# Optimization experiments

Hardware: AMD Instinct MI355X
Metric: run time of the kernel (lower is better)

## Reference

```python
import jax, jax.numpy as jnp
import numpy as np

EPS = 1e-6
H = 16  # heads

def rmsnorm(x, w):
    return x * jax.lax.rsqrt(jnp.mean(x * x, axis=-1, keepdims=True) + EPS) * w

def l2norm(x):
    return x * jax.lax.rsqrt(jnp.sum(x * x, axis=-1, keepdims=True) + EPS)

def setup_inputs() -> dict:
    key = jax.random.key(0)
    ks = jax.random.split(key, 12)
    B, S, D, F = 2, 2048, 1024, 4096
    std = 0.02
    inp = {
        'hidden_states': jax.random.normal(ks[0], (B, S, D), jnp.float32),
        'Wq': jax.random.normal(ks[1], (D, D), jnp.float32) * std,
        'Wk': jax.random.normal(ks[2], (D, D), jnp.float32) * std,
        'Wv': jax.random.normal(ks[3], (D, D), jnp.float32) * std,
        'Wb': jax.random.normal(ks[4], (D, H), jnp.float32) * std,
        'Wo': jax.random.normal(ks[5], (D, D), jnp.float32) * std,
        'ln1': jnp.ones((D,), jnp.float32),
        'ln2': jnp.ones((D,), jnp.float32),
        'Wg': jax.random.normal(ks[6], (D, F), jnp.float32) * std,
        'Wu': jax.random.normal(ks[7], (D, F), jnp.float32) * std,
        'Wd': jax.random.normal(ks[8], (F, D), jnp.float32) * std,
    }
    return inp

def delta_rule(q, k, v, beta):
    # q,k: [B,S,H,dk] (l2-normalized), v: [B,S,H,dv], beta: [B,S,H]
    B, S, Hh, dk = q.shape
    dv = v.shape[-1]
    # time-major for scan: [S,B,H,...]
    qt = jnp.moveaxis(q, 1, 0)
    kt = jnp.moveaxis(k, 1, 0)
    vt = jnp.moveaxis(v, 1, 0)
    bt = jnp.moveaxis(beta, 1, 0)

    def step(Sm, inp):
        qi, ki, vi, bi = inp  # [B,H,dk],[B,H,dk],[B,H,dv],[B,H]
        Sk = jnp.einsum('bhkv,bhk->bhv', Sm, ki)          # S^T k
        upd = ki[..., :, None] * (vi - Sk)[..., None, :]  # outer(k, v - S^T k)
        Sm = Sm + bi[..., None, None] * upd
        oi = jnp.einsum('bhkv,bhk->bhv', Sm, qi)
        return Sm, oi

    S0 = jnp.zeros((B, Hh, dk, dv), q.dtype)
    _, out = jax.lax.scan(step, S0, (qt, kt, vt, bt))
    return jnp.moveaxis(out, 0, 1)  # [B,S,H,dv]

def reference(hidden_states, Wq, Wk, Wv, Wb, Wo, ln1, ln2, Wg, Wu, Wd):
    B, S, D = hidden_states.shape
    dk = D // H
    # --- delta-rule attention sub-block ---
    x = rmsnorm(hidden_states, ln1)
    q = l2norm(jax.nn.silu(x @ Wq).reshape(B, S, H, dk))
    k = l2norm(jax.nn.silu(x @ Wk).reshape(B, S, H, dk))
    v = jax.nn.silu(x @ Wv).reshape(B, S, H, dk)
    beta = jax.nn.sigmoid(x @ Wb)  # [B,S,H]
    o = delta_rule(q, k, v, beta).reshape(B, S, D)
    h = hidden_states + o @ Wo
    # --- SwiGLU MLP sub-block ---
    y = rmsnorm(h, ln2)
    h = h + (jax.nn.silu(y @ Wg) * (y @ Wu)) @ Wd
    return h
```

## Files before the change

### kernel.cpp

```cpp
#include <hip/hip_runtime.h>
#include <hip/hip_bf16.h>
#include <stdint.h>

#define BB 2
#define SS 2048
#define DD 1024
#define FF 4096
#define HH 16
#define ROWS (BB*SS)
#define NC 32
#define NQKV 3200

typedef float f32x4 __attribute__((ext_vector_type(4)));
typedef __bf16 bf16x8 __attribute__((ext_vector_type(8)));

typedef __attribute__((address_space(1))) const void* gas1p;
typedef __attribute__((address_space(3))) void* las3p;

__device__ __forceinline__ void gload16(const void* g, void* l) {
    __builtin_amdgcn_global_load_lds((gas1p)g, (las3p)l, 16, 0, 0);
}

__device__ __forceinline__ unsigned short f2bf(float f) {
    unsigned int u = __builtin_bit_cast(unsigned int, f);
    u += 0x7fffu + ((u >> 16) & 1u);
    return (unsigned short)(u >> 16);
}
__device__ __forceinline__ float bf2f(unsigned short s) {
    unsigned int u = ((unsigned int)s) << 16;
    return __builtin_bit_cast(float, u);
}
__device__ __forceinline__ float sigmoidf_(float x) { return 1.f / (1.f + __expf(-x)); }
__device__ __forceinline__ float siluf_(float x)    { return x / (1.f + __expf(-x)); }

__device__ __forceinline__ int swz(int b) { return b ^ (((b >> 7) & 7) << 4); }

__device__ __forceinline__ void tp_body(const float* __restrict__ W,
                                        unsigned short* __restrict__ Wt,
                                        int K, int N, int bx, int by, int tid) {
    __shared__ float tile[32][33];
    int tx = tid & 31, ty = tid >> 5;
    int n0 = bx * 32, k0 = by * 32;
#pragma unroll
    for (int i = 0; i < 4; ++i)
        tile[ty + 8 * i][tx] = W[(size_t)(k0 + ty + 8 * i) * N + n0 + tx];
    __syncthreads();
#pragma unroll
    for (int i = 0; i < 4; ++i)
        Wt[(size_t)(n0 + ty + 8 * i) * K + k0 + tx] = f2bf(tile[tx][ty + 8 * i]);
}

__global__ __launch_bounds__(256) void transpose_cvt(const float* __restrict__ W,
                                                     unsigned short* __restrict__ Wt,
                                                     int K, int N) {
    tp_body(W, Wt, K, N, blockIdx.x, blockIdx.y, threadIdx.x);
}

__global__ __launch_bounds__(256) void transpose_cvt4(const float* W0, const float* W1,
                                                      const float* W2, const float* W3,
                                                      unsigned short* T0, unsigned short* T1,
                                                      unsigned short* T2, unsigned short* T3) {
    const float* W = (blockIdx.z == 0) ? W0 : (blockIdx.z == 1) ? W1 : (blockIdx.z == 2) ? W2 : W3;
    unsigned short* T = (blockIdx.z == 0) ? T0 : (blockIdx.z == 1) ? T1 : (blockIdx.z == 2) ? T2 : T3;
    tp_body(W, T, DD, DD, blockIdx.x, blockIdx.y, threadIdx.x);
}

__global__ __launch_bounds__(256) void transpose_cvt_gu(const float* W0, const float* W1,
                                                        unsigned short* Wt) {
    const float* W = (blockIdx.z == 0) ? W0 : W1;
    int isU = blockIdx.z;
    __shared__ float tile[32][33];
    int tid = threadIdx.x;
    int tx = tid & 31, ty = tid >> 5;
    int n0 = blockIdx.x * 32, k0 = blockIdx.y * 32;
#pragma unroll
    for (int i = 0; i < 4; ++i)
        tile[ty + 8 * i][tx] = W[(size_t)(k0 + ty + 8 * i) * FF + n0 + tx];
    __syncthreads();
#pragma unroll
    for (int i = 0; i < 4; ++i) {
        int j = n0 + ty + 8 * i;
        int rint = ((j >> 4) << 5) + (j & 15) + (isU << 4);
        Wt[(size_t)rint * DD + k0 + tx] = f2bf(tile[tx][ty + 8 * i]);
    }
}

__global__ __launch_bounds__(256) void wbt_kernel(const float* __restrict__ Wb,
                                                  unsigned short* __restrict__ WbT) {
    int idx = blockIdx.x * 256 + threadIdx.x;
    int d = idx >> 4, h = idx & 15;
    WbT[h * DD + d] = f2bf(Wb[idx]);
}

__global__ __launch_bounds__(256) void rmsnorm_bf16_kernel(const float* __restrict__ src,
                                                           const float* __restrict__ w,
                                                           unsigned short* __restrict__ dst) {
    int row = blockIdx.x;
    int tid = threadIdx.x;
    float4 x = ((const float4*)(src + (size_t)row * DD))[tid];
    float ss = x.x * x.x + x.y * x.y + x.z * x.z + x.w * x.w;
#pragma unroll
    for (int m = 1; m < 64; m <<= 1) ss += __shfl_xor(ss, m, 64);
    __shared__ float ws4[4];
    if ((tid & 63) == 0) ws4[tid >> 6] = ss;
    __syncthreads();
    ss = ws4[0] + ws4[1] + ws4[2] + ws4[3];
    float sc = rsqrtf(ss * (1.f / DD) + 1e-6f);
    float4 wv = ((const float4*)w)[tid];
    ushort4 o;
    o.x = f2bf(x.x * sc * wv.x);
    o.y = f2bf(x.y * sc * wv.y);
    o.z = f2bf(x.z * sc * wv.z);
    o.w = f2bf(x.w * sc * wv.w);
    ((ushort4*)(dst + (size_t)row * DD))[tid] = o;
}

template <int EP, int BMt, int BNt, int WM, int WN, bool FASTM>
__global__ __launch_bounds__(WM * WN * 64) void gemm2(const unsigned short* __restrict__ A,
                                                      const unsigned short* __restrict__ Bt,
                                                      const float* __restrict__ res,
                                                      float* __restrict__ cf,
                                                      unsigned short* __restrict__ cb,
                                                      int M, int N, int K) {
    constexpr int NW = WM * WN;
    constexpr int MI = BMt / (WM * 16);
    constexpr int NI = BNt / (WN * 16);
    constexpr int ACH = BMt / 8 / NW;
    constexpr int BCH = BNt / 8 / NW;
    constexpr int ABYTES = BMt * 128;
    constexpr int BBYTES = BNt * 128;
    __shared__ __align__(16) char lds[2 * (ABYTES + BBYTES)];

    int tid = threadIdx.x, lane = tid & 63, w = tid >> 6;
    int wm = w / WN, wn = w % WN;

    int gm = M / BMt, gn = N / BNt, nwg = gm * gn;
    int flat = blockIdx.x;
    int q = nwg >> 3, r8 = nwg & 7;
    int xcd = flat & 7, loc = flat >> 3;
    int sid = (xcd < r8 ? xcd * (q + 1) : r8 * (q + 1) + (xcd - r8) * q) + loc;
    int midx, nidx;
    if (FASTM) { midx = sid % gm; nidx = sid / gm; }
    else       { nidx = sid % gn; midx = sid / gn; }
    int m0 = midx * BMt, n0 = nidx * BNt;

    auto stage = [&](int buf, int kt) {
        char* base = (char*)lds + buf * (ABYTES + BBYTES);
        int row8 = lane >> 3, col = (lane & 7) * 8;
#pragma unroll
        for (int i = 0; i < ACH; ++i) {
            int c = w * ACH + i;
            gload16(A + ((size_t)(m0 + c * 8 + row8) * K + kt * 64 + col), base + c * 1024);
        }
#pragma unroll
        for (int i = 0; i < BCH; ++i) {
            int c = w * BCH + i;
            gload16(Bt + ((size_t)(n0 + c * 8 + row8) * K + kt * 64 + col), base + ABYTES + c * 1024);
        }
    };

    f32x4 acc[MI][NI] = {};
    int nk = K / 64;
    stage(0, 0);
    __syncthreads();
    int cur = 0;
    for (int kt = 0; kt < nk; ++kt) {
        if (kt + 1 < nk) stage(cur ^ 1, kt + 1);
        const char* abuf = (const char*)lds + cur * (ABYTES + BBYTES);
        const char* bbuf = abuf + ABYTES;
#pragma unroll
        for (int kk = 0; kk < 2; ++kk) {
            bf16x8 afr[MI], bfr[NI];
#pragma unroll
            for (int mi = 0; mi < MI; ++mi)
                afr[mi] = *(const bf16x8*)(abuf + (wm * (MI * 16) + mi * 16 + (lane & 15)) * 128 + kk * 64 + (lane >> 4) * 16);
#pragma unroll
            for (int ni = 0; ni < NI; ++ni)
                bfr[ni] = *(const bf16x8*)(bbuf + (wn * (NI * 16) + ni * 16 + (lane & 15)) * 128 + kk * 64 + (lane >> 4) * 16);
#pragma unroll
            for (int mi = 0; mi < MI; ++mi)
#pragma unroll
                for (int ni = 0; ni < NI; ++ni)
                    acc[mi][ni] = __builtin_amdgcn_mfma_f32_16x16x32_bf16(afr[mi], bfr[ni], acc[mi][ni], 0, 0, 0);
        }
        if (kt + 1 < nk) {
            __syncthreads();
            cur ^= 1;
        }
    }

    int mbase = m0 + wm * (MI * 16) + (lane >> 4) * 4;
    int nbase = n0 + wn * (NI * 16) + (lane & 15);
#pragma unroll
    for (int mi = 0; mi < MI; ++mi)
#pragma unroll
        for (int ni = 0; ni < NI; ++ni)
#pragma unroll
            for (int r = 0; r < 4; ++r) {
                int m = mbase + mi * 16 + r;
                int n = nbase + ni * 16;
                float v = acc[mi][ni][r];
                if (EP == 3) {
                    int seg = n >> 10, col = n & 1023;
                    if (seg < 3)
                        cb[(size_t)seg * ROWS * DD + (size_t)m * DD + col] = f2bf(v);
                    else if (col < 16)
                        cf[(size_t)m * HH + col] = sigmoidf_(v);
                } else {
                    if (EP == 1) v += res[(size_t)m * N + n];
                    if (EP == 2) cb[(size_t)m * N + n] = f2bf(v);
                    else         cf[(size_t)m * N + n] = v;
                }
            }
}

__global__ __launch_bounds__(512, 2) void gemm8_gu(const unsigned short* __restrict__ A,
                                                   const unsigned short* __restrict__ Bt,
                                                   unsigned short* __restrict__ cb,
                                                   int M, int N, int K) {
    __shared__ __align__(16) char lds8[4 * 32768];
    int tid = threadIdx.x, lane = tid & 63, w = tid >> 6;
    int wm = w >> 2, wn = w & 3;

    int gm = M / 256, gn = N / 256, nwg = gm * gn;
    int flat = blockIdx.x;
    int q = nwg >> 3, r8 = nwg & 7;
    int xcd = flat & 7, loc = flat >> 3;
    int sid = (xcd < r8 ? xcd * (q + 1) : r8 * (q + 1) + (xcd - r8) * q) + loc;
    int midx = sid % gm, nidx = sid / gm;
    int m0 = midx * 256, n0 = nidx * 256;

    int rl = tid >> 2;
    int sc = ((tid & 3) ^ (rl & 3)) * 8;
    auto stA = [&](int kt) {
        char* dst = lds8 + (kt & 3) * 32768;
        const unsigned short* src = A + (size_t)(m0 + rl) * K + kt * 32 + sc;
        gload16(src, dst + tid * 16);
        gload16(src + (size_t)128 * K, dst + 8192 + tid * 16);
    };
    auto stB = [&](int kt) {
        char* dst = lds8 + (kt & 3) * 32768 + 16384;
        const unsigned short* src = Bt + (size_t)(n0 + rl) * K + kt * 32 + sc;
        gload16(src, dst + tid * 16);
        gload16(src + (size_t)128 * K, dst + 8192 + tid * 16);
    };
    auto rdA = [&](const char* Ab, int mi) -> bf16x8 {
        int b = (wm * 128 + mi * 16 + (lane & 15)) * 64 + (lane >> 4) * 16;
        return *(const bf16x8*)(Ab + (b ^ (((b >> 6) & 3) << 4)));
    };
    auto rdB = [&](const char* Bb, int ni) -> bf16x8 {
        int b = (wn * 64 + ni * 16 + (lane & 15)) * 64 + (lane >> 4) * 16;
        return *(const bf16x8*)(Bb + (b ^ (((b >> 6) & 3) << 4)));
    };

    f32x4 acc[8][4] = {};
    int nk = K / 32;

    stA(0); stB(0); stA(1); stB(1); stA(2); stB(2);

    for (int kt = 0; kt < nk; ++kt) {
        int rem = nk - 1 - kt;
        if (rem >= 2)      asm volatile("s_waitcnt vmcnt(8)" ::: "memory");
        else if (rem == 1) asm volatile("s_waitcnt vmcnt(4)" ::: "memory");
        else               asm volatile("s_waitcnt vmcnt(0)" ::: "memory");
        __builtin_amdgcn_s_barrier();
        __builtin_amdgcn_sched_barrier(0);
        const char* Ab = lds8 + (kt & 3) * 32768;
        const char* Bb = Ab + 16384;

        bf16x8 bfr[4];
        {
            bf16x8 af[4];
#pragma unroll
            for (int mi = 0; mi < 4; ++mi) af[mi] = rdA(Ab, mi);
#pragma unroll
            for (int ni = 0; ni < 4; ++ni) bfr[ni] = rdB(Bb, ni);
            if (kt + 3 < nk) stA(kt + 3);
            __builtin_amdgcn_s_barrier();
            __builtin_amdgcn_s_setprio(1);
#pragma unroll
            for (int mi = 0; mi < 4; ++mi)
#pragma unroll
                for (int ni = 0; ni < 4; ++ni)
                    acc[mi][ni] = __builtin_amdgcn_mfma_f32_16x16x32_bf16(af[mi], bfr[ni], acc[mi][ni], 0, 0, 0);
            __builtin_amdgcn_s_setprio(0);
            __builtin_amdgcn_s_barrier();
        }
        {
            bf16x8 af[4];
#pragma unroll
            for (int mi = 0; mi < 4; ++mi) af[mi] = rdA(Ab, mi + 4);
            if (kt + 3 < nk) stB(kt + 3);
            __builtin_amdgcn_s_barrier();
            __builtin_amdgcn_s_setprio(1);
#pragma unroll
            for (int mi = 0; mi < 4; ++mi)
#pragma unroll
                for (int ni = 0; ni < 4; ++ni)
                    acc[mi + 4][ni] = __builtin_amdgcn_mfma_f32_16x16x32_bf16(af[mi], bfr[ni], acc[mi + 4][ni], 0, 0, 0);
            __builtin_amdgcn_s_setprio(0);
        }
    }

    int j0 = (n0 + wn * 64) / 2 + (lane & 15);
    int mb = m0 + wm * 128 + (lane >> 4) * 4;
#pragma unroll
    for (int mi = 0; mi < 8; ++mi)
#pragma unroll
        for (int p = 0; p < 2; ++p)
#pragma unroll
            for (int r = 0; r < 4; ++r) {
                int m = mb + mi * 16 + r;
                float gv = acc[mi][2 * p][r], uv = acc[mi][2 * p + 1][r];
                cb[(size_t)m * FF + j0 + 16 * p] = f2bf(siluf_(gv) * uv);
            }
}


__device__ __forceinline__ bf16x8 ldsfrag(const char* mat, int row, int kt, int lane) {
    return *(const bf16x8*)(mat + swz(row * 128 + kt * 64 + (lane >> 4) * 16));
}

template <bool INIT_P>
__device__ __forceinline__ void mm64(const char* X, const char* Y, const char* P,
                                     f32x4 acc[4], int w, int lane) {
    int g = lane >> 4;
#pragma unroll
    for (int j = 0; j < 4; ++j) {
        if (INIT_P) {
#pragma unroll
            for (int r = 0; r < 4; ++r) {
                int m = 16 * w + g * 4 + r, n = (lane & 15) + 16 * j;
                acc[j][r] = bf2f(*(const unsigned short*)(P + swz(m * 128 + n * 2)));
            }
        } else {
            acc[j] = (f32x4){0.f, 0.f, 0.f, 0.f};
        }
    }
    bf16x8 xs0 = ldsfrag(X, 16 * w + (lane & 15), 0, lane);
    bf16x8 xs1 = ldsfrag(X, 16 * w + (lane & 15), 1, lane);
#pragma unroll
    for (int j = 0; j < 4; ++j) {
        bf16x8 y0 = ldsfrag(Y, 16 * j + (lane & 15), 0, lane);
        bf16x8 y1 = ldsfrag(Y, 16 * j + (lane & 15), 1, lane);
        acc[j] = __builtin_amdgcn_mfma_f32_16x16x32_bf16(xs0, y0, acc[j], 0, 0, 0);
        acc[j] = __builtin_amdgcn_mfma_f32_16x16x32_bf16(xs1, y1, acc[j], 0, 0, 0);
    }
}

__device__ __forceinline__ void wR(char* D, const f32x4 acc[4], int w, int lane, int mode) {
    int g = lane >> 4;
#pragma unroll
    for (int j = 0; j < 4; ++j)
#pragma unroll
        for (int r = 0; r < 4; ++r) {
            int m = 16 * w + g * 4 + r, n = (lane & 15) + 16 * j;
            float v = acc[j][r];
            if (mode >= 1) v = (n < m) ? v : 0.f;
            if (mode == 2) v = ((m == n) ? 1.f : 0.f) - v;
            *(unsigned short*)(D + swz(m * 128 + n * 2)) = f2bf(v);
        }
}

__device__ __forceinline__ void wT(char* D, const f32x4 acc[4], int w, int lane, int mode) {
    int g = lane >> 4;
#pragma unroll
    for (int j = 0; j < 4; ++j) {
        int n = (lane & 15) + 16 * j, m0 = 16 * w + g * 4;
        ushort4 pk;
        pk.x = (mode == 1 && !(n < m0 + 0)) ? (unsigned short)0 : f2bf(acc[j][0]);
        pk.y = (mode == 1 && !(n < m0 + 1)) ? (unsigned short)0 : f2bf(acc[j][1]);
        pk.z = (mode == 1 && !(n < m0 + 2)) ? (unsigned short)0 : f2bf(acc[j][2]);
        pk.w = (mode == 1 && !(n < m0 + 3)) ? (unsigned short)0 : f2bf(acc[j][3]);
        *(ushort4*)(D + swz(n * 128 + m0 * 2)) = pk;
    }
}

__device__ __forceinline__ void load16bf(const unsigned short* p, float* v) {
    uint4 a = *(const uint4*)p, b = *(const uint4*)(p + 8);
    unsigned int u0[8] = {a.x, a.y, a.z, a.w, b.x, b.y, b.z, b.w};
#pragma unroll
    for (int i = 0; i < 8; ++i) {
        v[2 * i]     = bf2f((unsigned short)(u0[i] & 0xffffu));
        v[2 * i + 1] = bf2f((unsigned short)(u0[i] >> 16));
    }
}

__global__ __launch_bounds__(256) void delta_prep_kernel(const unsigned short* __restrict__ qb,
                                                         const unsigned short* __restrict__ kb,
                                                         const unsigned short* __restrict__ vb,
                                                         const float* __restrict__ betab,
                                                         char* __restrict__ chunkbuf) {
    __shared__ __align__(16) char sK[8192], sKb[8192], sKbT[8192], sVbT[8192], sQ[8192];
    __shared__ __align__(16) char mA[8192], mAT[8192], mB2[8192], mBT[8192], mP0[8192], mP1[8192];

    int ci = blockIdx.x;
    int c = ci & 31, h = (ci >> 5) & 15, b = ci >> 9;
    int tid = threadIdx.x;
    int lane = tid & 63, w = tid >> 6;

    char* cbuf = chunkbuf + (size_t)ci * 40960;
    unsigned short* Qg  = (unsigned short*)(cbuf);
    unsigned short* KTg = (unsigned short*)(cbuf + 8192);
    unsigned short* Ag  = (unsigned short*)(cbuf + 16384);
    unsigned short* Wg  = (unsigned short*)(cbuf + 24576);
    unsigned short* U0g = (unsigned short*)(cbuf + 32768);

    {
        int trow = tid >> 2, part = tid & 3, d0 = part * 16;
        size_t rg = (size_t)b * SS + c * 64 + trow;
        float bet = betab[rg * HH + h];
        size_t base = rg * DD + h * 64 + d0;

        float qv[16], kv[16], vv[16];
        load16bf(qb + base, qv);
        load16bf(kb + base, kv);
        load16bf(vb + base, vv);

        float ssq = 0.f, ssk = 0.f;
#pragma unroll
        for (int i = 0; i < 16; ++i) {
            qv[i] = siluf_(qv[i]); ssq += qv[i] * qv[i];
            kv[i] = siluf_(kv[i]); ssk += kv[i] * kv[i];
            vv[i] = siluf_(vv[i]);
        }
        ssq += __shfl_xor(ssq, 1, 64); ssq += __shfl_xor(ssq, 2, 64);
        ssk += __shfl_xor(ssk, 1, 64); ssk += __shfl_xor(ssk, 2, 64);
        float scq = rsqrtf(ssq + 1e-6f), sck = rsqrtf(ssk + 1e-6f);
#pragma unroll
        for (int i = 0; i < 16; ++i) { qv[i] *= scq; kv[i] *= sck; }

#pragma unroll
        for (int m = 0; m < 4; ++m) {
            ushort4 pq, pk_, pkb;
#pragma unroll
            for (int r = 0; r < 4; ++r) {
                ((unsigned short*)&pq)[r]  = f2bf(qv[4 * m + r]);
                ((unsigned short*)&pk_)[r] = f2bf(kv[4 * m + r]);
                ((unsigned short*)&pkb)[r] = f2bf(bet * kv[4 * m + r]);
            }
            int bo = trow * 128 + (d0 + 4 * m) * 2;
            *(ushort4*)(sQ + swz(bo))  = pq;
            *(ushort4*)(sK + swz(bo))  = pk_;
            *(ushort4*)(sKb + swz(bo)) = pkb;
            *(ushort4*)(Qg + trow * 64 + d0 + 4 * m) = pq;
        }
#pragma unroll
        for (int e = 0; e < 16; ++e) {
            int d = d0 + e;
            *(unsigned short*)(sKbT + swz(d * 128 + trow * 2)) = f2bf(bet * kv[e]);
            *(unsigned short*)(sVbT + swz(d * 128 + trow * 2)) = f2bf(bet * vv[e]);
            KTg[d * 64 + trow] = f2bf(kv[e]);
        }
    }
    __syncthreads();

    f32x4 acc[4];
    mm64<false>(sKb, sK, nullptr, acc, w, lane);
    wR(mA, acc, w, lane, 1);
    wT(mAT, acc, w, lane, 1);
    wR(mP0, acc, w, lane, 2);
    __syncthreads();

    char *cX = mA, *cXT = mAT, *nX = mB2, *nXT = mBT, *pc = mP0, *pn = mP1;
#pragma unroll
    for (int s = 0; s < 5; ++s) {
        mm64<false>(cX, cXT, nullptr, acc, w, lane);
        wR(nX, acc, w, lane, 0);
        wT(nXT, acc, w, lane, 0);
        __syncthreads();
        mm64<true>(pc, nXT, pc, acc, w, lane);
        wR(pn, acc, w, lane, 0);
        __syncthreads();
        char* t;
        t = cX; cX = nX; nX = t;
        t = cXT; cXT = nXT; nXT = t;
        t = pc; pc = pn; pn = t;
    }

    int g = lane >> 4;
    mm64<false>(sK, sQ, nullptr, acc, w, lane);
#pragma unroll
    for (int j = 0; j < 4; ++j) {
        int n = (lane & 15) + 16 * j, m0 = 16 * w + g * 4;
        ushort4 pk;
        pk.x = (m0 + 0 <= n) ? f2bf(acc[j][0]) : (unsigned short)0;
        pk.y = (m0 + 1 <= n) ? f2bf(acc[j][1]) : (unsigned short)0;
        pk.z = (m0 + 2 <= n) ? f2bf(acc[j][2]) : (unsigned short)0;
        pk.w = (m0 + 3 <= n) ? f2bf(acc[j][3]) : (unsigned short)0;
        *(ushort4*)(Ag + n * 64 + m0) = pk;
    }
    mm64<false>(sKbT, pc, nullptr, acc, w, lane);
#pragma unroll
    for (int j = 0; j < 4; ++j) {
        int n = (lane & 15) + 16 * j, m0 = 16 * w + g * 4;
        ushort4 pk;
        pk.x = f2bf(acc[j][0]); pk.y = f2bf(acc[j][1]);
        pk.z = f2bf(acc[j][2]); pk.w = f2bf(acc[j][3]);
        *(ushort4*)(Wg + n * 64 + m0) = pk;
    }
    mm64<false>(pc, sVbT, nullptr, acc, w, lane);
#pragma unroll
    for (int j = 0; j < 4; ++j) {
        int n = (lane & 15) + 16 * j, m0 = 16 * w + g * 4;
        ushort4 pk;
        pk.x = f2bf(acc[j][0]); pk.y = f2bf(acc[j][1]);
        pk.z = f2bf(acc[j][2]); pk.w = f2bf(acc[j][3]);
        *(ushort4*)(U0g + n * 64 + m0) = pk;
    }
}

__global__ __launch_bounds__(256) void delta_seq_kernel(const char* __restrict__ chunkbuf,
                                                        unsigned short* __restrict__ ob) {
    __shared__ __align__(16) char stg[2 * 40960 + 8192 + 8192];
    int bh = blockIdx.x;
    int b = bh >> 4, h = bh & 15;
    int tid = threadIdx.x;
    int lane = tid & 63, w = tid >> 6, g = lane >> 4;

    char* UTw = stg + 81920 + w * 2048;
    char* Slw = stg + 90112 + w * 2048;

    f32x4 s_acc[4];
#pragma unroll
    for (int j = 0; j < 4; ++j) s_acc[j] = (f32x4){0.f, 0.f, 0.f, 0.f};
    uint4 z4 = {0, 0, 0, 0};
    *(uint4*)(Slw + lane * 32) = z4;
    *(uint4*)(Slw + lane * 32 + 16) = z4;

    const char* cbase = chunkbuf + (size_t)bh * NC * 40960;
    int lo = (lane * 16) ^ ((lane >> 3) << 4);
    int pw = 10 * w;

    {
        const char* src = cbase;
        char* dst = stg;
#pragma unroll
        for (int p = 0; p < 10; ++p)
            gload16(src + (pw + p) * 1024 + lo, dst + (pw + p) * 1024);
    }

    for (int c = 0; c < NC; ++c) {
        {
            const char* src = cbase + (size_t)((c + 1) & 31) * 40960;
            char* dst = stg + ((c + 1) & 1) * 40960;
#pragma unroll
            for (int p = 0; p < 10; ++p)
                gload16(src + (pw + p) * 1024 + lo, dst + (pw + p) * 1024);
        }
        asm volatile("s_waitcnt vmcnt(10)" ::: "memory");
        __builtin_amdgcn_s_barrier();
        __builtin_amdgcn_sched_barrier(0);

        const char* cur = stg + (c & 1) * 40960;
        const char* Qm = cur, *KTm = cur + 8192, *Am = cur + 16384, *Wm = cur + 24576, *U0m = cur + 32768;

        bf16x8 xs0 = ldsfrag(Slw, lane & 15, 0, lane);
        bf16x8 xs1 = ldsfrag(Slw, lane & 15, 1, lane);

        f32x4 ut[4];
        f32x4 oa[4];
#pragma unroll
        for (int j = 0; j < 4; ++j) { ut[j] = (f32x4){0.f, 0.f, 0.f, 0.f}; oa[j] = (f32x4){0.f, 0.f, 0.f, 0.f}; }
#pragma unroll
        for (int j = 0; j < 4; ++j) {
            bf16x8 y0 = ldsfrag(Wm, 16 * j + (lane & 15), 0, lane);
            bf16x8 y1 = ldsfrag(Wm, 16 * j + (lane & 15), 1, lane);
            ut[j] = __builtin_amdgcn_mfma_f32_16x16x32_bf16(xs0, y0, ut[j], 0, 0, 0);
            ut[j] = __builtin_amdgcn_mfma_f32_16x16x32_bf16(xs1, y1, ut[j], 0, 0, 0);
        }
#pragma unroll
        for (int j = 0; j < 4; ++j) {
            bf16x8 y0 = ldsfrag(Qm, 16 * j + (lane & 15), 0, lane);
            bf16x8 y1 = ldsfrag(Qm, 16 * j + (lane & 15), 1, lane);
            oa[j] = __builtin_amdgcn_mfma_f32_16x16x32_bf16(xs0, y0, oa[j], 0, 0, 0);
            oa[j] = __builtin_amdgcn_mfma_f32_16x16x32_bf16(xs1, y1, oa[j], 0, 0, 0);
        }
#pragma unroll
        for (int j = 0; j < 4; ++j)
#pragma unroll
            for (int r = 0; r < 4; ++r) {
                int m = 16 * w + g * 4 + r;
                int n = (lane & 15) + 16 * j;
                float u0 = bf2f(*(const unsigned short*)(U0m + swz(m * 128 + n * 2)));
                float u = u0 - ut[j][r];
                *(unsigned short*)(UTw + swz((g * 4 + r) * 128 + n * 2)) = f2bf(u);
            }
        bf16x8 us0 = ldsfrag(UTw, lane & 15, 0, lane);
        bf16x8 us1 = ldsfrag(UTw, lane & 15, 1, lane);
#pragma unroll
        for (int j = 0; j < 4; ++j) {
            bf16x8 y0 = ldsfrag(Am, 16 * j + (lane & 15), 0, lane);
            bf16x8 y1 = ldsfrag(Am, 16 * j + (lane & 15), 1, lane);
            oa[j] = __builtin_amdgcn_mfma_f32_16x16x32_bf16(us0, y0, oa[j], 0, 0, 0);
            oa[j] = __builtin_amdgcn_mfma_f32_16x16x32_bf16(us1, y1, oa[j], 0, 0, 0);
        }
#pragma unroll
        for (int j = 0; j < 4; ++j) {
            bf16x8 y0 = ldsfrag(KTm, 16 * j + (lane & 15), 0, lane);
            bf16x8 y1 = ldsfrag(KTm, 16 * j + (lane & 15), 1, lane);
            s_acc[j] = __builtin_amdgcn_mfma_f32_16x16x32_bf16(us0, y0, s_acc[j], 0, 0, 0);
            s_acc[j] = __builtin_amdgcn_mfma_f32_16x16x32_bf16(us1, y1, s_acc[j], 0, 0, 0);
        }
#pragma unroll
        for (int j = 0; j < 4; ++j) {
            int n = (lane & 15) + 16 * j;
            size_t tg = (size_t)b * SS + c * 64 + n;
            int col = h * 64 + 16 * w + g * 4;
            ushort4 pk;
            pk.x = f2bf(oa[j][0]); pk.y = f2bf(oa[j][1]);
            pk.z = f2bf(oa[j][2]); pk.w = f2bf(oa[j][3]);
            *(ushort4*)(ob + tg * DD + col) = pk;
        }
#pragma unroll
        for (int j = 0; j < 4; ++j)
#pragma unroll
            for (int r = 0; r < 4; ++r) {
                int n = (lane & 15) + 16 * j;
                *(unsigned short*)(Slw + swz((g * 4 + r) * 128 + n * 2)) = f2bf(s_acc[j][r]);
            }

        asm volatile("" ::: "memory");
        __builtin_amdgcn_s_barrier();
        __builtin_amdgcn_sched_barrier(0);
    }
}

extern "C" void kernel_launch(void* const* d_in, const int* in_sizes, int n_in,
                              void* d_out, int out_size, void* d_ws, size_t ws_size,
                              hipStream_t stream) {
    const float* hidden = (const float*)d_in[0];
    const float* Wq  = (const float*)d_in[1];
    const float* Wk  = (const float*)d_in[2];
    const float* Wv  = (const float*)d_in[3];
    const float* Wb  = (const float*)d_in[4];
    const float* Wo  = (const float*)d_in[5];
    const float* ln1 = (const float*)d_in[6];
    const float* ln2 = (const float*)d_in[7];
    const float* Wg  = (const float*)d_in[8];
    const float* Wu  = (const float*)d_in[9];
    const float* Wd  = (const float*)d_in[10];
    float* out = (float*)d_out;
    char* ws = (char*)d_ws;

    const size_t MB = 1024 * 1024;
    const size_t KB256 = 262144;
    unsigned short* wq_t = (unsigned short*)(ws + 0 * MB);
    unsigned short* wk_t = (unsigned short*)(ws + 2 * MB);
    unsigned short* wv_t = (unsigned short*)(ws + 4 * MB);
    unsigned short* wbT  = (unsigned short*)(ws + 6 * MB);
    unsigned short* wo_t = (unsigned short*)(ws + 6 * MB + KB256);
    unsigned short* btGU = (unsigned short*)(ws + 8 * MB + KB256);
    unsigned short* wd_t = (unsigned short*)(ws + 24 * MB + KB256);
    float* hbuf          = (float*)(ws + 32 * MB + KB256);
    unsigned short* yb   = (unsigned short*)(ws + 48 * MB + KB256);
    unsigned short* qb   = (unsigned short*)(ws + 56 * MB + KB256);
    unsigned short* kb   = (unsigned short*)(ws + 64 * MB + KB256);
    unsigned short* vb   = (unsigned short*)(ws + 72 * MB + KB256);
    float* betab         = (float*)(ws + 80 * MB + KB256);
    unsigned short* xb   = (unsigned short*)(ws + 80 * MB + 2 * KB256);
    unsigned short* ob   = xb;
    char* chunkbuf       = ws + 88 * MB + 2 * KB256;
    unsigned short* act  = (unsigned short*)(ws + 56 * MB + KB256);

    dim3 blk(256);

    transpose_cvt4<<<dim3(32, 32, 4), blk, 0, stream>>>(Wq, Wk, Wv, Wo, wq_t, wk_t, wv_t, wo_t);
    transpose_cvt_gu<<<dim3(128, 32, 2), blk, 0, stream>>>(Wg, Wu, btGU);
    transpose_cvt<<<dim3(32, 128), blk, 0, stream>>>(Wd, wd_t, FF, DD);
    wbt_kernel<<<64, blk, 0, stream>>>(Wb, wbT);

    rmsnorm_bf16_kernel<<<ROWS, blk, 0, stream>>>(hidden, ln1, xb);

    gemm2<3, 128, 128, 2, 2, false><<<dim3((NQKV / 128) * (ROWS / 128)), blk, 0, stream>>>(
        xb, wq_t, nullptr, betab, qb, ROWS, NQKV, DD);

    delta_prep_kernel<<<1024, blk, 0, stream>>>(qb, kb, vb, betab, chunkbuf);
    delta_seq_kernel<<<BB * HH, blk, 0, stream>>>(chunkbuf, ob);

    gemm2<1, 128, 128, 2, 2, false><<<dim3((DD / 128) * (ROWS / 128)), blk, 0, stream>>>(
        ob, wo_t, hidden, hbuf, nullptr, ROWS, DD, DD);

    rmsnorm_bf16_kernel<<<ROWS, blk, 0, stream>>>(hbuf, ln2, yb);

    gemm8_gu<<<dim3((ROWS / 256) * (2 * FF / 256)), dim3(512), 0, stream>>>(
        yb, btGU, act, ROWS, 2 * FF, DD);

    gemm2<1, 128, 128, 2, 2, false><<<dim3((DD / 128) * (ROWS / 128)), blk, 0, stream>>>(
        act, wd_t, hbuf, out, nullptr, ROWS, DD, FF);
}
```

Before: 456.1 us.

## Generalize 256-row MFMA GEMM and use it for QKV and split-K down projection

Turns the gate/up GEMM kernel into a template over tile width, epilogue and split-K count. The QKV+beta projection now runs through it with 256x128 tiles. The down projection runs as a 2-way split-K with 256x128 tiles, writing fp32 partials that a new elementwise kernel sums together with the residual. The LDS swizzle pattern also changes. This raises per-block reuse and adds parallelism for the long-K down projection, at the cost of an extra partial-buffer write and read plus one more launch.

```diff
diff --git a/kernel.cpp b/kernel.cpp
--- a/kernel.cpp
+++ b/kernel.cpp
@@ -200,122 +200,174 @@
                 int m = mbase + mi * 16 + r;
                 int n = nbase + ni * 16;
                 float v = acc[mi][ni][r];
-                if (EP == 3) {
+                if (EP == 1) v += res[(size_t)m * N + n];
+                if (EP == 2) cb[(size_t)m * N + n] = f2bf(v);
+                else         cf[(size_t)m * N + n] = v;
+            }
+}
+
+template <int EP, int BN, int SPLIT>
+__global__ __launch_bounds__(512, 2) void gemm8(const unsigned short* __restrict__ A,
+                                                const unsigned short* __restrict__ Bt,
+                                                float* __restrict__ cf,
+                                                unsigned short* __restrict__ cb,
+                                                int M, int N, int K) {
+    constexpr int NI = BN / 64;
+    constexpr int SLOT = 16384 + BN * 64;
+    constexpr int LPT = 2 + (BN == 256 ? 2 : 1);
+    __shared__ __align__(16) char lds8[4 * SLOT];
+    int tid = threadIdx.x, lane = tid & 63, w = tid >> 6;
+    int wm = w >> 2, wn = w & 3;
+
+    int gm = M / 256, gn = N / BN, nwg = gm * gn * SPLIT;
+    int flat = blockIdx.x;
+    int q = nwg >> 3, r8 = nwg & 7;
+    int xcd = flat & 7, loc = flat >> 3;
+    int sid = (xcd < r8 ? xcd * (q + 1) : r8 * (q + 1) + (xcd - r8) * q) + loc;
+    int split = 0;
+    if (SPLIT > 1) { split = sid / (gm * gn); sid -= split * gm * gn; }
+    int midx = sid % gm, nidx = sid / gm;
+    int m0 = midx * 256, n0 = nidx * BN;
+
+    int nkl = (K / SPLIT) / 32;
+    int kt0 = split * nkl;
+
+    int rl = tid >> 2;
+    int sc = ((tid & 3) ^ ((rl >> 1) & 3)) * 8;
+    auto stA = [&](int t) {
+        char* dst = lds8 + (t & 3) * SLOT;
+        const unsigned short* src = A + (size_t)(m0 + rl) * K + t * 32 + sc;
+        gload16(src, dst + tid * 16);
+        gload16(src + (size_t)128 * K, dst + 8192 + tid * 16);
+    };
+    auto stB = [&](int t) {
+        char* dst = lds8 + (t & 3) * SLOT + 16384;
+        const unsigned short* src = Bt + (size_t)(n0 + rl) * K + t * 32 + sc;
+        gload16(src, dst + tid * 16);
+        if constexpr (BN == 256) gload16(src + (size_t)128 * K, dst + 8192 + tid * 16);
+    };
+    auto rdA = [&](const char* Ab, int mi) -> bf16x8 {
+        int b = (wm * 128 + mi * 16 + (lane & 15)) * 64 + (lane >> 4) * 16;
+        return *(const bf16x8*)(Ab + (b ^ (((b >> 7) & 3) << 4)));
+    };
+    auto rdB = [&](const char* Bb, int ni) -> bf16x8 {
+        int b = (wn * (BN / 4) + ni * 16 + (lane & 15)) * 64 + (lane >> 4) * 16;
+        return *(const bf16x8*)(Bb + (b ^ (((b >> 7) & 3) << 4)));
+    };
+
+    f32x4 acc[8][NI] = {};
+
+    stA(kt0); stB(kt0); stA(kt0 + 1); stB(kt0 + 1); stA(kt0 + 2); stB(kt0 + 2);
+
+    for (int t = 0; t < nkl; ++t) {
+        int ktg = kt0 + t;
+        int rem = nkl - 1 - t;
+        if (rem >= 2) {
+            if constexpr (LPT == 4) asm volatile("s_waitcnt vmcnt(8)" ::: "memory");
+            else                    asm volatile("s_waitcnt vmcnt(6)" ::: "memory");
+        } else if (rem == 1) {
+            if constexpr (LPT == 4) asm volatile("s_waitcnt vmcnt(4)" ::: "memory");
+            else                    asm volatile("s_waitcnt vmcnt(3)" ::: "memory");
+        } else {
+            asm volatile("s_waitcnt vmcnt(0)" ::: "memory");
+        }
+        __builtin_amdgcn_s_barrier();
+        __builtin_amdgcn_sched_barrier(0);
+        const char* Ab = lds8 + (ktg & 3) * SLOT;
+        const char* Bb = Ab + 16384;
+
+        bf16x8 bfr[NI];
+        {
+            bf16x8 af[4];
+#pragma unroll
+            for (int mi = 0; mi < 4; ++mi) af[mi] = rdA(Ab, mi);
+#pragma unroll
+            for (int ni = 0; ni < NI; ++ni) bfr[ni] = rdB(Bb, ni);
+            if (t + 3 < nkl) stA(ktg + 3);
+            __builtin_amdgcn_s_barrier();
+            __builtin_amdgcn_s_setprio(1);
+#pragma unroll
+            for (int mi = 0; mi < 4; ++mi)
+#pragma unroll
+                for (int ni = 0; ni < NI; ++ni)
+                    acc[mi][ni] = __builtin_amdgcn_mfma_f32_16x16x32_bf16(af[mi], bfr[ni], acc[mi][ni], 0, 0, 0);
+            __builtin_amdgcn_s_setprio(0);
+            __builtin_amdgcn_s_barrier();
+        }
+        {
+            bf16x8 af[4];
+#pragma unroll
+            for (int mi = 0; mi < 4; ++mi) af[mi] = rdA(Ab, mi + 4);
+            if (t + 3 < nkl) stB(ktg + 3);
+            __builtin_amdgcn_s_barrier();
+            __builtin_amdgcn_s_setprio(1);
+#pragma unroll
+            for (int mi = 0; mi < 4; ++mi)
+#pragma unroll
+                for (int ni = 0; ni < NI; ++ni)
+                    acc[mi + 4][ni] = __builtin_amdgcn_mfma_f32_16x16x32_bf16(af[mi], bfr[ni], acc[mi + 4][ni], 0, 0, 0);
+            __builtin_amdgcn_s_setprio(0);
+        }
+    }
+
+    int mb = m0 + wm * 128 + (lane >> 4) * 4;
+    if constexpr (EP == 4) {
+        int j0 = (n0 + wn * (BN / 4)) / 2 + (lane & 15);
+#pragma unroll
+        for (int mi = 0; mi < 8; ++mi)
+#pragma unroll
+            for (int p = 0; p < NI / 2; ++p)
+#pragma unroll
+                for (int r = 0; r < 4; ++r) {
+                    int m = mb + mi * 16 + r;
+                    float gv = acc[mi][2 * p][r], uv = acc[mi][2 * p + 1][r];
+                    cb[(size_t)m * FF + j0 + 16 * p] = f2bf(siluf_(gv) * uv);
+                }
+    } else if constexpr (EP == 3) {
+        int nb = n0 + wn * (BN / 4) + (lane & 15);
+#pragma unroll
+        for (int mi = 0; mi < 8; ++mi)
+#pragma unroll
+            for (int ni = 0; ni < NI; ++ni)
+#pragma unroll
+                for (int r = 0; r < 4; ++r) {
+                    int m = mb + mi * 16 + r;
+                    int n = nb + ni * 16;
+                    float v = acc[mi][ni][r];
                     int seg = n >> 10, col = n & 1023;
                     if (seg < 3)
                         cb[(size_t)seg * ROWS * DD + (size_t)m * DD + col] = f2bf(v);
                     else if (col < 16)
                         cf[(size_t)m * HH + col] = sigmoidf_(v);
-                } else {
-                    if (EP == 1) v += res[(size_t)m * N + n];
-                    if (EP == 2) cb[(size_t)m * N + n] = f2bf(v);
-                    else         cf[(size_t)m * N + n] = v;
                 }
-            }
-}
-
-__global__ __launch_bounds__(512, 2) void gemm8_gu(const unsigned short* __restrict__ A,
-                                                   const unsigned short* __restrict__ Bt,
-                                                   unsigned short* __restrict__ cb,
-                                                   int M, int N, int K) {
-    __shared__ __align__(16) char lds8[4 * 32768];
-    int tid = threadIdx.x, lane = tid & 63, w = tid >> 6;
-    int wm = w >> 2, wn = w & 3;
-
-    int gm = M / 256, gn = N / 256, nwg = gm * gn;
-    int flat = blockIdx.x;
-    int q = nwg >> 3, r8 = nwg & 7;
-    int xcd = flat & 7, loc = flat >> 3;
-    int sid = (xcd < r8 ? xcd * (q + 1) : r8 * (q + 1) + (xcd - r8) * q) + loc;
-    int midx = sid % gm, nidx = sid / gm;
-    int m0 = midx * 256, n0 = nidx * 256;
-
-    int rl = tid >> 2;
-    int sc = ((tid & 3) ^ (rl & 3)) * 8;
-    auto stA = [&](int kt) {
-        char* dst = lds8 + (kt & 3) * 32768;
-        const unsigned short* src = A + (size_t)(m0 + rl) * K + kt * 32 + sc;
-        gload16(src, dst + tid * 16);
-        gload16(src + (size_t)128 * K, dst + 8192 + tid * 16);
-    };
-    auto stB = [&](int kt) {
-        char* dst = lds8 + (kt & 3) * 32768 + 16384;
-        const unsigned short* src = Bt + (size_t)(n0 + rl) * K + kt * 32 + sc;
-        gload16(src, dst + tid * 16);
-        gload16(src + (size_t)128 * K, dst + 8192 + tid * 16);
-    };
-    auto rdA = [&](const char* Ab, int mi) -> bf16x8 {
-        int b = (wm * 128 + mi * 16 + (lane & 15)) * 64 + (lane >> 4) * 16;
-        return *(const bf16x8*)(Ab + (b ^ (((b >> 6) & 3) << 4)));
-    };
-    auto rdB = [&](const char* Bb, int ni) -> bf16x8 {
-        int b = (wn * 64 + ni * 16 + (lane & 15)) * 64 + (lane >> 4) * 16;
-        return *(const bf16x8*)(Bb + (b ^ (((b >> 6) & 3) << 4)));
-    };
-
-    f32x4 acc[8][4] = {};
-    int nk = K / 32;
-
-    stA(0); stB(0); stA(1); stB(1); stA(2); stB(2);
-
-    for (int kt = 0; kt < nk; ++kt) {
-        int rem = nk - 1 - kt;
-        if (rem >= 2)      asm volatile("s_waitcnt vmcnt(8)" ::: "memory");
-        else if (rem == 1) asm volatile("s_waitcnt vmcnt(4)" ::: "memory");
-        else               asm volatile("s_waitcnt vmcnt(0)" ::: "memory");
-        __builtin_amdgcn_s_barrier();
-        __builtin_amdgcn_sched_barrier(0);
-        const char* Ab = lds8 + (kt & 3) * 32768;
-        const char* Bb = Ab + 16384;
-
-        bf16x8 bfr[4];
-        {
-            bf16x8 af[4];
-#pragma unroll
-            for (int mi = 0; mi < 4; ++mi) af[mi] = rdA(Ab, mi);
-#pragma unroll
-            for (int ni = 0; ni < 4; ++ni) bfr[ni] = rdB(Bb, ni);
-            if (kt + 3 < nk) stA(kt + 3);
-            __builtin_amdgcn_s_barrier();
-            __builtin_amdgcn_s_setprio(1);
-#pragma unroll
-            for (int mi = 0; mi < 4; ++mi)
-#pragma unroll
-                for (int ni = 0; ni < 4; ++ni)
-                    acc[mi][ni] = __builtin_amdgcn_mfma_f32_16x16x32_bf16(af[mi], bfr[ni], acc[mi][ni], 0, 0, 0);
-            __builtin_amdgcn_s_setprio(0);
-            __builtin_amdgcn_s_barrier();
-        }
-        {
-            bf16x8 af[4];
-#pragma unroll
-            for (int mi = 0; mi < 4; ++mi) af[mi] = rdA(Ab, mi + 4);
-            if (kt + 3 < nk) stB(kt + 3);
-            __builtin_amdgcn_s_barrier();
-            __builtin_amdgcn_s_setprio(1);
-#pragma unroll
-            for (int mi = 0; mi < 4; ++mi)
-#pragma unroll
-                for (int ni = 0; ni < 4; ++ni)
-                    acc[mi + 4][ni] = __builtin_amdgcn_mfma_f32_16x16x32_bf16(af[mi], bfr[ni], acc[mi + 4][ni], 0, 0, 0);
-            __builtin_amdgcn_s_setprio(0);
-        }
-    }
-
-    int j0 = (n0 + wn * 64) / 2 + (lane & 15);
-    int mb = m0 + wm * 128 + (lane >> 4) * 4;
-#pragma unroll
-    for (int mi = 0; mi < 8; ++mi)
-#pragma unroll
-        for (int p = 0; p < 2; ++p)
-#pragma unroll
-            for (int r = 0; r < 4; ++r) {
-                int m = mb + mi * 16 + r;
-                float gv = acc[mi][2 * p][r], uv = acc[mi][2 * p + 1][r];
-                cb[(size_t)m * FF + j0 + 16 * p] = f2bf(siluf_(gv) * uv);
-            }
-}
-
+    } else {
+        int nb = n0 + wn * (BN / 4) + (lane & 15);
+        float* dst = cf + (size_t)split * M * N;
+#pragma unroll
+        for (int mi = 0; mi < 8; ++mi)
+#pragma unroll
+            for (int ni = 0; ni < NI; ++ni)
+#pragma unroll
+                for (int r = 0; r < 4; ++r)
+                    dst[(size_t)(mb + mi * 16 + r) * N + nb + ni * 16] = acc[mi][ni][r];
+    }
+}
+
+__global__ void wd_reduce_kernel(const float* __restrict__ p, const float* __restrict__ res,
+                                 float* __restrict__ out) {
+    const int n4 = ROWS * DD / 4;
+    int i = blockIdx.x * 256 + threadIdx.x;
+    int stride = gridDim.x * 256;
+    const float4* p0 = (const float4*)p;
+    const float4* p1 = (const float4*)(p + (size_t)ROWS * DD);
+    const float4* r4 = (const float4*)res;
+    float4* o4 = (float4*)out;
+    for (; i < n4; i += stride) {
+        float4 a = r4[i], b = p0[i], c = p1[i];
+        a.x += b.x + c.x; a.y += b.y + c.y; a.z += b.z + c.z; a.w += b.w + c.w;
+        o4[i] = a;
+    }
+}
 
 __device__ __forceinline__ bf16x8 ldsfrag(const char* mat, int row, int kt, int lane) {
     return *(const bf16x8*)(mat + swz(row * 128 + kt * 64 + (lane >> 4) * 16));
@@ -662,6 +714,7 @@
     unsigned short* ob   = xb;
     char* chunkbuf       = ws + 88 * MB + 2 * KB256;
     unsigned short* act  = (unsigned short*)(ws + 56 * MB + KB256);
+    float* pbuf          = (float*)chunkbuf;
 
     dim3 blk(256);
 
@@ -672,8 +725,7 @@
 
     rmsnorm_bf16_kernel<<<ROWS, blk, 0, stream>>>(hidden, ln1, xb);
 
-    gemm2<3, 128, 128, 2, 2, false><<<dim3((NQKV / 128) * (ROWS / 128)), blk, 0, stream>>>(
-        xb, wq_t, nullptr, betab, qb, ROWS, NQKV, DD);
+    gemm8<3, 128, 1><<<dim3(400), dim3(512), 0, stream>>>(xb, wq_t, betab, qb, ROWS, NQKV, DD);
 
     delta_prep_kernel<<<1024, blk, 0, stream>>>(qb, kb, vb, betab, chunkbuf);
     delta_seq_kernel<<<BB * HH, blk, 0, stream>>>(chunkbuf, ob);
@@ -683,9 +735,8 @@
 
     rmsnorm_bf16_kernel<<<ROWS, blk, 0, stream>>>(hbuf, ln2, yb);
 
-    gemm8_gu<<<dim3((ROWS / 256) * (2 * FF / 256)), dim3(512), 0, stream>>>(
-        yb, btGU, act, ROWS, 2 * FF, DD);
-
-    gemm2<1, 128, 128, 2, 2, false><<<dim3((DD / 128) * (ROWS / 128)), blk, 0, stream>>>(
-        act, wd_t, hbuf, out, nullptr, ROWS, DD, FF);
-}
+    gemm8<4, 256, 1><<<dim3(512), dim3(512), 0, stream>>>(yb, btGU, nullptr, act, ROWS, 2 * FF, DD);
+
+    gemm8<0, 128, 2><<<dim3(256), dim3(512), 0, stream>>>(act, wd_t, pbuf, nullptr, ROWS, DD, FF);
+    wd_reduce_kernel<<<2048, 256, 0, stream>>>(pbuf, hbuf, out);
+}
```

Result: slower. 467.3 us (+2.5%).
